# Kernel optimization log

Hardware: AMD Instinct MI355X
Metric: run time of the kernel (lower is better)

## Reference

```python
import jax, jax.numpy as jnp
import numpy as np

# Static problem structure (matches setup_inputs)
B, NPOLY, VPP, L = 32, 256, 64, 32
LAYERS = 3
PLEN = L * 2 ** LAYERS  # 256
LN_EPS = 1e-5


def _layernorm(h, g, b):
    mu = h.mean(-1, keepdims=True)
    var = ((h - mu) ** 2).mean(-1, keepdims=True)
    return g * (h - mu) / jnp.sqrt(var + LN_EPS) + b


def _forward(data, W0, b0, g0, beta0, W1, b1, g1, beta1, W2, b2, g2, beta2,
             Wq, bq, Wk, bk, Wv, bv):
    # row 0 holds agent polyline index in feature 0
    agent_id = data[:, 0, 0].astype(jnp.int32)  # [B]
    vecs = data[:, 1:, :]
    vecs = vecs.at[:, :, -1].set(0.0)  # zero out polyline-id feature (data[:,:,-1]=0)
    x = vecs.reshape(B, NPOLY, VPP, L)  # uniform polyline groups

    # SubGraph: 3 layers of (MLP -> maxpool aggregate -> concat), doubling width
    for (W, b, g, be) in ((W0, b0, g0, beta0), (W1, b1, g1, beta1), (W2, b2, g2, beta2)):
        h = jax.nn.relu(_layernorm(x @ W + b, g, be))  # [B,P,V,c]
        agg = h.max(axis=2, keepdims=True)             # [B,P,1,c]
        x = jnp.concatenate([h, jnp.broadcast_to(agg, h.shape)], axis=-1)  # [B,P,V,2c]
    P = x.max(axis=2)  # [B, NPOLY, PLEN] polyline features

    # Global graph: single-head attention with agent polyline as query
    q = P[jnp.arange(B), agent_id] @ Wq + bq          # [B, C]
    k = P @ Wk + bk                                    # [B, P, C]
    v = P @ Wv + bv
    scores = jnp.einsum('bc,bpc->bp', q, k) / jnp.sqrt(jnp.float32(PLEN))
    att = jax.nn.softmax(scores, axis=-1)
    return jnp.einsum('bp,bpc->bc', att, v)           # [B, PLEN]


def setup_inputs() -> dict:
    key = jax.random.key(0)
    ks = jax.random.split(key, 24)
    V = 1 + NPOLY * VPP
    data = jax.random.normal(ks[0], (B, V, L), dtype=jnp.float32)
    agent = jax.random.randint(ks[1], (B,), 0, NPOLY).astype(jnp.float32)
    data = data.at[:, 0, :].set(0.0).at[:, 0, 0].set(agent)
    pid = jnp.repeat(jnp.arange(NPOLY), VPP).astype(jnp.float32)
    data = data.at[:, 1:, -1].set(pid[None, :])

    inp = {'data': data}
    c = L
    for i in range(LAYERS):
        inp[f'W{i}'] = 0.02 * jax.random.normal(ks[2 + i], (c, c), dtype=jnp.float32)
        inp[f'b{i}'] = jnp.zeros((c,), jnp.float32)
        inp[f'g{i}'] = jnp.ones((c,), jnp.float32)
        inp[f'beta{i}'] = jnp.zeros((c,), jnp.float32)
        c *= 2
    C = PLEN
    for j, nm in enumerate(('q', 'k', 'v')):
        inp[f'W{nm}'] = 0.02 * jax.random.normal(ks[10 + j], (C, C), dtype=jnp.float32)
        inp[f'b{nm}'] = jnp.zeros((C,), jnp.float32)
    return inp


def reference(data, W0, b0, g0, beta0, W1, b1, g1, beta1, W2, b2, g2, beta2,
              Wq, bq, Wk, bk, Wv, bv):
    return _forward(data, W0, b0, g0, beta0, W1, b1, g1, beta1, W2, b2, g2, beta2,
                    Wq, bq, Wk, bk, Wv, bv)
```

## Files before the change

kernel.cpp:

```cpp
#include <hip/hip_runtime.h>

#define NPOLY 256
#define VPP   64
#define LCH   32
#define NV    (1 + NPOLY * VPP)
#define LN_EPS 1e-5f

typedef __bf16 bf16x8 __attribute__((ext_vector_type(8)));
typedef float  f32x4  __attribute__((ext_vector_type(4)));

union U4B8 { uint4 u; bf16x8 v; };

__device__ __forceinline__ unsigned packbf(float a, float b) {
    unsigned r;
    asm("v_cvt_pk_bf16_f32 %0, %1, %2" : "=v"(r) : "v"(a), "v"(b));
    return r;
}

#define DPPF(x, ctrl) __int_as_float(__builtin_amdgcn_update_dpp(0, __float_as_int(x), (ctrl), 0xF, 0xF, true))

__device__ __forceinline__ float red16sum(float x) {
    x += DPPF(x, 0xB1);
    x += DPPF(x, 0x4E);
    x += DPPF(x, 0x141);
    x += DPPF(x, 0x140);
    return x;
}

__global__ void vn_prep(const float* __restrict__ W0, const float* __restrict__ W1,
                        const float* __restrict__ W2,
                        const float* __restrict__ Wq, const float* __restrict__ Wk,
                        const float* __restrict__ Wv,
                        float* __restrict__ Wvf, float* __restrict__ Wqf,
                        float* __restrict__ WkfT, uint4* __restrict__ wpack)
{
    int t = blockIdx.x * 256 + threadIdx.x;
    if (t < 32768) {
        Wvf[t] = Wv[t] + Wv[t + 32768];
        return;
    }
    t -= 32768;
    if (t < 32768) {
        Wqf[t] = Wq[t] + Wq[t + 32768];
        return;
    }
    t -= 32768;
    if (t < 32768) {
        int j = t >> 8, c = t & 255;
        WkfT[c * 128 + j] = Wk[j * 256 + c] + Wk[(j + 128) * 256 + c];
        return;
    }
    t -= 32768;
    if (t < 22 * 64) {
        int f = t >> 6, L = t & 63, q = L >> 4, m = L & 15;
        const float* src; int N, k0, col;
        if (f < 2)      { src = W0; N = 32;  k0 = q * 8;                 col = f * 16 + m; }
        else if (f < 6) { src = W1; N = 64;  k0 = q * 8;                 col = (f - 2) * 16 + m; }
        else { int g = f - 6; src = W2; N = 128; k0 = (g >> 3) * 32 + q * 8; col = (g & 7) * 16 + m; }
        float e[8];
        #pragma unroll
        for (int j = 0; j < 8; j++) e[j] = src[(k0 + j) * N + col];
        uint4 o;
        o.x = packbf(e[0], e[1]); o.y = packbf(e[2], e[3]);
        o.z = packbf(e[4], e[5]); o.w = packbf(e[6], e[7]);
        wpack[f * 64 + L] = o;
    }
}

__global__ __launch_bounds__(256, 3) void vn_mlp(
    const float* __restrict__ data, const uint4* __restrict__ wpack,
    const float* __restrict__ b0, const float* __restrict__ g0, const float* __restrict__ be0,
    const float* __restrict__ W1, const float* __restrict__ b1,
    const float* __restrict__ g1, const float* __restrict__ be1,
    const float* __restrict__ W2, const float* __restrict__ b2,
    const float* __restrict__ g2, const float* __restrict__ be2,
    float* __restrict__ Ph)
{
    __shared__ __align__(16) unsigned short hbuf[64 * 72];
    __shared__ float partA[4][128];
    __shared__ float partB[4][128];

    const int tid = threadIdx.x;
    const int w = tid >> 6, L = tid & 63, q = L >> 4, m = L & 15;
    const int blk = blockIdx.x;
    const int bb = blk >> 8, pp = blk & 255;
    const int r0 = w * 16;

    const float* rowbase = data + ((size_t)bb * NV + 1 + (size_t)pp * VPP) * LCH;
    bf16x8 A0;
    {
        const float* rp = rowbase + (size_t)(r0 + m) * LCH + q * 8;
        float4 u = *(const float4*)rp;
        float4 v = *(const float4*)(rp + 4);
        if (q == 3) v.w = 0.f;
        U4B8 c;
        c.u.x = packbf(u.x, u.y); c.u.y = packbf(u.z, u.w);
        c.u.z = packbf(v.x, v.y); c.u.w = packbf(v.z, v.w);
        A0 = c.v;
    }
    f32x4 acc0[2];
    {
        U4B8 t0, t1; t0.u = wpack[0 * 64 + L]; t1.u = wpack[1 * 64 + L];
        float bca = b0[m], bcb = b0[16 + m];
        f32x4 a0 = { bca, bca, bca, bca };
        f32x4 a1 = { bcb, bcb, bcb, bcb };
        acc0[0] = __builtin_amdgcn_mfma_f32_16x16x32_bf16(A0, t0.v, a0, 0, 0, 0);
        acc0[1] = __builtin_amdgcn_mfma_f32_16x16x32_bf16(A0, t1.v, a1, 0, 0, 0);
    }
    {
        float g0c[2]  = { g0[m],  g0[16 + m]  };
        float be0c[2] = { be0[m], be0[16 + m] };
        float a0mx[2] = { 0.f, 0.f };
        #pragma unroll
        for (int reg = 0; reg < 4; reg++) {
            float x0 = acc0[0][reg], x1 = acc0[1][reg];
            float rs = red16sum(x0 + x1);
            float rq = red16sum(x0 * x0 + x1 * x1);
            float mu = rs * (1.f / 32.f);
            float var = rq * (1.f / 32.f) - mu * mu;
            float ri = rsqrtf(var + LN_EPS);
            #pragma unroll
            for (int ct = 0; ct < 2; ct++) {
                float v = fmaxf(fmaf(g0c[ct] * ri, acc0[ct][reg] - mu, be0c[ct]), 0.f);
                acc0[ct][reg] = v;
                a0mx[ct] = fmaxf(a0mx[ct], v);
            }
        }
        #pragma unroll
        for (int ct = 0; ct < 2; ct++) {
            float v = a0mx[ct];
            v = fmaxf(v, __shfl_xor(v, 16, 64));
            v = fmaxf(v, __shfl_xor(v, 32, 64));
            a0mx[ct] = v;
        }
        if (q == 0) { partA[w][m] = a0mx[0]; partA[w][16 + m] = a0mx[1]; }
    }
    #pragma unroll
    for (int reg = 0; reg < 4; reg++) {
        int row = r0 + q * 4 + reg;
        unsigned u = packbf(acc0[0][reg], acc0[1][reg]);
        hbuf[row * 72 + m]      = (unsigned short)u;
        hbuf[row * 72 + 16 + m] = (unsigned short)(u >> 16);
    }
    __syncthreads();

    {
        float p = 0.f;
        int j0 = w * 8;
        #pragma unroll
        for (int jj = 0; jj < 8; jj++) {
            int j = j0 + jj;
            float a = fmaxf(fmaxf(partA[0][j], partA[1][j]), fmaxf(partA[2][j], partA[3][j]));
            p = fmaf(a, W1[(32 + j) * 64 + L], p);
        }
        partB[w][L] = p;
    }
    __syncthreads();

    bf16x8 A1;
    { U4B8 c; c.u = *(const uint4*)(hbuf + (r0 + m) * 72 + q * 8); A1 = c.v; }
    f32x4 acc1[4];
    #pragma unroll
    for (int ct = 0; ct < 4; ct++) {
        U4B8 wv; wv.u = wpack[(2 + ct) * 64 + L];
        int n = ct * 16 + m;
        float au = b1[n] + ((partB[0][n] + partB[1][n]) + (partB[2][n] + partB[3][n]));
        f32x4 a = { au, au, au, au };
        acc1[ct] = __builtin_amdgcn_mfma_f32_16x16x32_bf16(A1, wv.v, a, 0, 0, 0);
    }
    {
        float g1c[4], be1c[4];
        #pragma unroll
        for (int ct = 0; ct < 4; ct++) { g1c[ct] = g1[ct * 16 + m]; be1c[ct] = be1[ct * 16 + m]; }
        float a1mx[4] = { 0.f, 0.f, 0.f, 0.f };
        #pragma unroll
        for (int reg = 0; reg < 4; reg++) {
            float rs = 0.f, rq = 0.f;
            #pragma unroll
            for (int ct = 0; ct < 4; ct++) { float x = acc1[ct][reg]; rs += x; rq = fmaf(x, x, rq); }
            rs = red16sum(rs);
            rq = red16sum(rq);
            float mu = rs * (1.f / 64.f);
            float var = rq * (1.f / 64.f) - mu * mu;
            float ri = rsqrtf(var + LN_EPS);
            #pragma unroll
            for (int ct = 0; ct < 4; ct++) {
                float v = fmaxf(fmaf(g1c[ct] * ri, acc1[ct][reg] - mu, be1c[ct]), 0.f);
                acc1[ct][reg] = v;
                a1mx[ct] = fmaxf(a1mx[ct], v);
            }
        }
        #pragma unroll
        for (int ct = 0; ct < 4; ct++) {
            float v = a1mx[ct];
            v = fmaxf(v, __shfl_xor(v, 16, 64));
            v = fmaxf(v, __shfl_xor(v, 32, 64));
            a1mx[ct] = v;
        }
        if (q == 0) {
            #pragma unroll
            for (int ct = 0; ct < 4; ct++) partA[w][ct * 16 + m] = a1mx[ct];
        }
    }
    #pragma unroll
    for (int reg = 0; reg < 4; reg++) {
        int row = r0 + q * 4 + reg;
        unsigned ua = packbf(acc1[0][reg], acc1[1][reg]);
        unsigned ub = packbf(acc1[2][reg], acc1[3][reg]);
        hbuf[row * 72 + m]      = (unsigned short)ua;
        hbuf[row * 72 + 16 + m] = (unsigned short)(ua >> 16);
        hbuf[row * 72 + 32 + m] = (unsigned short)ub;
        hbuf[row * 72 + 48 + m] = (unsigned short)(ub >> 16);
    }
    __syncthreads();

    {
        float pa = 0.f, pb = 0.f;
        int j0 = w * 16;
        #pragma unroll
        for (int jj = 0; jj < 16; jj++) {
            int j = j0 + jj;
            float a = fmaxf(fmaxf(partA[0][j], partA[1][j]), fmaxf(partA[2][j], partA[3][j]));
            pa = fmaf(a, W2[(64 + j) * 128 + L],      pa);
            pb = fmaf(a, W2[(64 + j) * 128 + 64 + L], pb);
        }
        partB[w][L]      = pa;
        partB[w][64 + L] = pb;
    }
    __syncthreads();

    bf16x8 A2[2];
    #pragma unroll
    for (int ks = 0; ks < 2; ks++) {
        U4B8 c; c.u = *(const uint4*)(hbuf + (r0 + m) * 72 + ks * 32 + q * 8);
        A2[ks] = c.v;
    }
    f32x4 acc2[8];
    #pragma unroll
    for (int ct = 0; ct < 8; ct++) {
        U4B8 wa, wb;
        wa.u = wpack[(6 + ct) * 64 + L];
        wb.u = wpack[(14 + ct) * 64 + L];
        int n = ct * 16 + m;
        float au = b2[n] + ((partB[0][n] + partB[1][n]) + (partB[2][n] + partB[3][n]));
        f32x4 a = { au, au, au, au };
        a = __builtin_amdgcn_mfma_f32_16x16x32_bf16(A2[0], wa.v, a, 0, 0, 0);
        a = __builtin_amdgcn_mfma_f32_16x16x32_bf16(A2[1], wb.v, a, 0, 0, 0);
        acc2[ct] = a;
    }
    {
        float g2c[8], be2c[8];
        #pragma unroll
        for (int ct = 0; ct < 8; ct++) { g2c[ct] = g2[ct * 16 + m]; be2c[ct] = be2[ct * 16 + m]; }
        float m2[8] = { 0.f, 0.f, 0.f, 0.f, 0.f, 0.f, 0.f, 0.f };
        #pragma unroll
        for (int reg = 0; reg < 4; reg++) {
            float rs = 0.f, rq = 0.f;
            #pragma unroll
            for (int ct = 0; ct < 8; ct++) { float x = acc2[ct][reg]; rs += x; rq = fmaf(x, x, rq); }
            rs = red16sum(rs);
            rq = red16sum(rq);
            float mu = rs * (1.f / 128.f);
            float var = rq * (1.f / 128.f) - mu * mu;
            float ri = rsqrtf(var + LN_EPS);
            #pragma unroll
            for (int ct = 0; ct < 8; ct++) {
                float v = fmaxf(fmaf(g2c[ct] * ri, acc2[ct][reg] - mu, be2c[ct]), 0.f);
                m2[ct] = fmaxf(m2[ct], v);
            }
        }
        #pragma unroll
        for (int ct = 0; ct < 8; ct++) {
            float v = m2[ct];
            v = fmaxf(v, __shfl_xor(v, 16, 64));
            v = fmaxf(v, __shfl_xor(v, 32, 64));
            m2[ct] = v;
        }
        if (q == 0) {
            #pragma unroll
            for (int ct = 0; ct < 8; ct++) partA[w][ct * 16 + m] = m2[ct];
        }
    }
    __syncthreads();

    if (tid < 128) {
        float v = fmaxf(fmaxf(partA[0][tid], partA[1][tid]),
                        fmaxf(partA[2][tid], partA[3][tid]));
        Ph[(size_t)blk * 128 + tid] = v;
    }
}

__global__ __launch_bounds__(256) void vn_attn(
    const float* __restrict__ data, const float* __restrict__ Ph,
    const float* __restrict__ Wqf, const float* __restrict__ WkfT,
    const float* __restrict__ bq,
    const float* __restrict__ Wvf, const float* __restrict__ bv,
    float* __restrict__ out)
{
    extern __shared__ float shPh[];
    __shared__ __align__(16) float qs[256], tts[128], att[256], pb[128];
    __shared__ __align__(16) float part[256];
    __shared__ float red[8];
    const int b = blockIdx.x, tid = threadIdx.x, lane = tid & 63, wave = tid >> 6;
    const float* PhB = Ph + (size_t)b * NPOLY * 128;
    const int agent = (int)data[(size_t)b * NV * LCH];

    {
        const float4* src = (const float4*)PhB;
        #pragma unroll
        for (int it = 0; it < 32; it++) {
            int idx4 = it * 256 + tid;
            float4 v = src[idx4];
            int lin = idx4 * 4;
            int p = lin >> 7, c = lin & 127;
            float* dst = shPh + p * 129 + c;
            dst[0] = v.x; dst[1] = v.y; dst[2] = v.z; dst[3] = v.w;
        }
    }
    __syncthreads();

    {
        const int c = tid;
        const float* pa = shPh + agent * 129;
        float s0 = bq[c], s1 = 0.f, s2 = 0.f, s3 = 0.f;
        for (int i = 0; i < 128; i += 4) {
            s0 = fmaf(pa[i],     Wqf[(i)     * 256 + c], s0);
            s1 = fmaf(pa[i + 1], Wqf[(i + 1) * 256 + c], s1);
            s2 = fmaf(pa[i + 2], Wqf[(i + 2) * 256 + c], s2);
            s3 = fmaf(pa[i + 3], Wqf[(i + 3) * 256 + c], s3);
        }
        qs[c] = (s0 + s1) + (s2 + s3);
    }
    __syncthreads();

    {
        const int j = tid & 127, h = tid >> 7;
        const float* wk = WkfT + (size_t)(h * 128) * 128 + j;
        const float* qp = qs + h * 128;
        float s0 = 0.f, s1 = 0.f, s2 = 0.f, s3 = 0.f;
        for (int c = 0; c < 128; c += 4) {
            s0 = fmaf(qp[c],     wk[(c)     * 128], s0);
            s1 = fmaf(qp[c + 1], wk[(c + 1) * 128], s1);
            s2 = fmaf(qp[c + 2], wk[(c + 2) * 128], s2);
            s3 = fmaf(qp[c + 3], wk[(c + 3) * 128], s3);
        }
        part[tid] = (s0 + s1) + (s2 + s3);
    }
    __syncthreads();
    if (tid < 128) tts[tid] = part[tid] + part[128 + tid];
    __syncthreads();

    float sv;
    {
        const float* prl = shPh + tid * 129;
        float s0 = 0.f, s1 = 0.f, s2 = 0.f, s3 = 0.f;
        #pragma unroll
        for (int j = 0; j < 128; j += 4) {
            s0 = fmaf(prl[j],     tts[j],     s0);
            s1 = fmaf(prl[j + 1], tts[j + 1], s1);
            s2 = fmaf(prl[j + 2], tts[j + 2], s2);
            s3 = fmaf(prl[j + 3], tts[j + 3], s3);
        }
        sv = ((s0 + s1) + (s2 + s3)) * 0.0625f;
    }
    float mx = sv;
    #pragma unroll
    for (int s = 1; s < 64; s <<= 1) mx = fmaxf(mx, __shfl_xor(mx, s, 64));
    if (lane == 0) red[wave] = mx;
    __syncthreads();
    mx = fmaxf(fmaxf(red[0], red[1]), fmaxf(red[2], red[3]));
    float e = expf(sv - mx);
    float sm = e;
    #pragma unroll
    for (int s = 1; s < 64; s <<= 1) sm += __shfl_xor(sm, s, 64);
    if (lane == 0) red[4 + wave] = sm;
    __syncthreads();
    const float tot = red[4] + red[5] + red[6] + red[7];
    att[tid] = e / tot;
    __syncthreads();

    {
        const int c = tid & 127, h = tid >> 7;
        const float* ap = att + h * 128;
        const float* pp = shPh + (size_t)(h * 128) * 129 + c;
        float s0 = 0.f, s1 = 0.f, s2 = 0.f, s3 = 0.f;
        #pragma unroll
        for (int p = 0; p < 128; p += 4) {
            s0 = fmaf(ap[p],     pp[(p)     * 129], s0);
            s1 = fmaf(ap[p + 1], pp[(p + 1) * 129], s1);
            s2 = fmaf(ap[p + 2], pp[(p + 2) * 129], s2);
            s3 = fmaf(ap[p + 3], pp[(p + 3) * 129], s3);
        }
        part[tid] = (s0 + s1) + (s2 + s3);
    }
    __syncthreads();
    if (tid < 128) pb[tid] = part[tid] + part[128 + tid];
    __syncthreads();

    {
        const float* wv = Wvf + tid;
        float s0 = 0.f, s1 = 0.f, s2 = 0.f, s3 = 0.f;
        #pragma unroll
        for (int j = 0; j < 128; j += 4) {
            s0 = fmaf(pb[j],     wv[(j)     * 256], s0);
            s1 = fmaf(pb[j + 1], wv[(j + 1) * 256], s1);
            s2 = fmaf(pb[j + 2], wv[(j + 2) * 256], s2);
            s3 = fmaf(pb[j + 3], wv[(j + 3) * 256], s3);
        }
        out[(size_t)b * 256 + tid] = bv[tid] + ((s0 + s1) + (s2 + s3));
    }
}

extern "C" void kernel_launch(void* const* d_in, const int* in_sizes, int n_in,
                              void* d_out, int out_size, void* d_ws, size_t ws_size,
                              hipStream_t stream)
{
    const float* data = (const float*)d_in[0];
    const float* W0 = (const float*)d_in[1];
    const float* b0 = (const float*)d_in[2];
    const float* g0 = (const float*)d_in[3];
    const float* be0= (const float*)d_in[4];
    const float* W1 = (const float*)d_in[5];
    const float* b1 = (const float*)d_in[6];
    const float* g1 = (const float*)d_in[7];
    const float* be1= (const float*)d_in[8];
    const float* W2 = (const float*)d_in[9];
    const float* b2 = (const float*)d_in[10];
    const float* g2 = (const float*)d_in[11];
    const float* be2= (const float*)d_in[12];
    const float* Wq = (const float*)d_in[13];
    const float* bq = (const float*)d_in[14];
    const float* Wk = (const float*)d_in[15];
    const float* bk = (const float*)d_in[16];
    const float* Wv = (const float*)d_in[17];
    const float* bv = (const float*)d_in[18];
    (void)bk;

    char* wsb = (char*)d_ws;
    float* Ph    = (float*)(wsb);
    float* Wqf   = (float*)(wsb + 4194304);
    float* WkfT  = (float*)(wsb + 4325376);
    float* Wvf   = (float*)(wsb + 4456448);
    uint4* wpack = (uint4*)(wsb + 4653568);

    static int attn_attr_set = 0;
    if (!attn_attr_set) {
        hipFuncSetAttribute((const void*)vn_attn,
                            hipFuncAttributeMaxDynamicSharedMemorySize, 132096);
        attn_attr_set = 1;
    }

    vn_prep<<<390, 256, 0, stream>>>(W0, W1, W2, Wq, Wk, Wv, Wvf, Wqf, WkfT, wpack);
    vn_mlp<<<32 * NPOLY, 256, 0, stream>>>(data, wpack,
                                           b0, g0, be0,
                                           W1, b1, g1, be1,
                                           W2, b2, g2, be2, Ph);
    vn_attn<<<32, 256, 132096, stream>>>(data, Ph, Wqf, WkfT, bq, Wvf, bv, (float*)d_out);
}
```

Before: 189.9 us.

## Split attention kernel across 8 blocks per batch and precompute max aggregates

```diff
diff --git a/kernel.cpp b/kernel.cpp
--- a/kernel.cpp
+++ b/kernel.cpp
@@ -79,6 +79,7 @@
     __shared__ __align__(16) unsigned short hbuf[64 * 72];
     __shared__ float partA[4][128];
     __shared__ float partB[4][128];
+    __shared__ float agg0[32], agg1[64];
 
     const int tid = threadIdx.x;
     const int w = tid >> 6, L = tid & 63, q = L >> 4, m = L & 15;
@@ -143,6 +144,10 @@
         hbuf[row * 72 + 16 + m] = (unsigned short)(u >> 16);
     }
     __syncthreads();
+    if (tid < 32)
+        agg0[tid] = fmaxf(fmaxf(partA[0][tid], partA[1][tid]),
+                          fmaxf(partA[2][tid], partA[3][tid]));
+    __syncthreads();
 
     {
         float p = 0.f;
@@ -150,8 +155,7 @@
         #pragma unroll
         for (int jj = 0; jj < 8; jj++) {
             int j = j0 + jj;
-            float a = fmaxf(fmaxf(partA[0][j], partA[1][j]), fmaxf(partA[2][j], partA[3][j]));
-            p = fmaf(a, W1[(32 + j) * 64 + L], p);
+            p = fmaf(agg0[j], W1[(32 + j) * 64 + L], p);
         }
         partB[w][L] = p;
     }
@@ -213,6 +217,10 @@
         hbuf[row * 72 + 48 + m] = (unsigned short)(ub >> 16);
     }
     __syncthreads();
+    if (tid < 64)
+        agg1[tid] = fmaxf(fmaxf(partA[0][tid], partA[1][tid]),
+                          fmaxf(partA[2][tid], partA[3][tid]));
+    __syncthreads();
 
     {
         float pa = 0.f, pb = 0.f;
@@ -220,7 +228,7 @@
         #pragma unroll
         for (int jj = 0; jj < 16; jj++) {
             int j = j0 + jj;
-            float a = fmaxf(fmaxf(partA[0][j], partA[1][j]), fmaxf(partA[2][j], partA[3][j]));
+            float a = agg1[j];
             pa = fmaf(a, W2[(64 + j) * 128 + L],      pa);
             pb = fmaf(a, W2[(64 + j) * 128 + 64 + L], pb);
         }
@@ -301,7 +309,8 @@
     __shared__ __align__(16) float qs[256], tts[128], att[256], pb[128];
     __shared__ __align__(16) float part[256];
     __shared__ float red[8];
-    const int b = blockIdx.x, tid = threadIdx.x, lane = tid & 63, wave = tid >> 6;
+    const int bg = blockIdx.x, b = bg >> 3, g = bg & 7;
+    const int tid = threadIdx.x, lane = tid & 63, wave = tid >> 6;
     const float* PhB = Ph + (size_t)b * NPOLY * 128;
     const int agent = (int)data[(size_t)b * NV * LCH];
 
@@ -398,16 +407,23 @@
     __syncthreads();
 
     {
-        const float* wv = Wvf + tid;
-        float s0 = 0.f, s1 = 0.f, s2 = 0.f, s3 = 0.f;
-        #pragma unroll
-        for (int j = 0; j < 128; j += 4) {
-            s0 = fmaf(pb[j],     wv[(j)     * 256], s0);
-            s1 = fmaf(pb[j + 1], wv[(j + 1) * 256], s1);
-            s2 = fmaf(pb[j + 2], wv[(j + 2) * 256], s2);
-            s3 = fmaf(pb[j + 3], wv[(j + 3) * 256], s3);
-        }
-        out[(size_t)b * 256 + tid] = bv[tid] + ((s0 + s1) + (s2 + s3));
+        const int c32 = tid & 31, jg = tid >> 5;
+        const float* wv = Wvf + g * 32 + c32;
+        const int j0 = jg * 16;
+        float s0 = 0.f, s1 = 0.f;
+        #pragma unroll
+        for (int jj = 0; jj < 16; jj += 2) {
+            s0 = fmaf(pb[j0 + jj],     wv[(j0 + jj)     * 256], s0);
+            s1 = fmaf(pb[j0 + jj + 1], wv[(j0 + jj + 1) * 256], s1);
+        }
+        part[tid] = s0 + s1;
+    }
+    __syncthreads();
+    if (tid < 32) {
+        float s = bv[g * 32 + tid];
+        #pragma unroll
+        for (int k = 0; k < 8; k++) s += part[k * 32 + tid];
+        out[(size_t)b * 256 + g * 32 + tid] = s;
     }
 }
 
@@ -455,5 +471,5 @@
                                            b0, g0, be0,
                                            W1, b1, g1, be1,
                                            W2, b2, g2, be2, Ph);
-    vn_attn<<<32, 256, 132096, stream>>>(data, Ph, Wqf, WkfT, bq, Wvf, bv, (float*)d_out);
-}
+    vn_attn<<<32 * 8, 256, 132096, stream>>>(data, Ph, Wqf, WkfT, bq, Wvf, bv, (float*)d_out);
+}
```

New measurement: 189.2 us. Within noise of the previous version (-0.3%).

## Split attention kernel reductions across 1024 threads with partial sums

Applied to the files above, without the earlier changes.

```diff
diff --git a/kernel.cpp b/kernel.cpp
--- a/kernel.cpp
+++ b/kernel.cpp
@@ -290,7 +290,7 @@
     }
 }
 
-__global__ __launch_bounds__(256) void vn_attn(
+__global__ __launch_bounds__(1024) void vn_attn(
     const float* __restrict__ data, const float* __restrict__ Ph,
     const float* __restrict__ Wqf, const float* __restrict__ WkfT,
     const float* __restrict__ bq,
@@ -298,18 +298,18 @@
     float* __restrict__ out)
 {
     extern __shared__ float shPh[];
-    __shared__ __align__(16) float qs[256], tts[128], att[256], pb[128];
-    __shared__ __align__(16) float part[256];
+    __shared__ __align__(16) float qs[256], tts[128], att[256], pb[128], sc[256];
+    __shared__ __align__(16) float part[1024];
     __shared__ float red[8];
-    const int b = blockIdx.x, tid = threadIdx.x, lane = tid & 63, wave = tid >> 6;
+    const int b = blockIdx.x, tid = threadIdx.x;
     const float* PhB = Ph + (size_t)b * NPOLY * 128;
     const int agent = (int)data[(size_t)b * NV * LCH];
 
     {
         const float4* src = (const float4*)PhB;
         #pragma unroll
-        for (int it = 0; it < 32; it++) {
-            int idx4 = it * 256 + tid;
+        for (int it = 0; it < 8; it++) {
+            int idx4 = it * 1024 + tid;
             float4 v = src[idx4];
             int lin = idx4 * 4;
             int p = lin >> 7, c = lin & 127;
@@ -320,95 +320,126 @@
     __syncthreads();
 
     {
-        const int c = tid;
-        const float* pa = shPh + agent * 129;
-        float s0 = bq[c], s1 = 0.f, s2 = 0.f, s3 = 0.f;
-        for (int i = 0; i < 128; i += 4) {
-            s0 = fmaf(pa[i],     Wqf[(i)     * 256 + c], s0);
-            s1 = fmaf(pa[i + 1], Wqf[(i + 1) * 256 + c], s1);
-            s2 = fmaf(pa[i + 2], Wqf[(i + 2) * 256 + c], s2);
-            s3 = fmaf(pa[i + 3], Wqf[(i + 3) * 256 + c], s3);
-        }
-        qs[c] = (s0 + s1) + (s2 + s3);
-    }
-    __syncthreads();
-
-    {
-        const int j = tid & 127, h = tid >> 7;
-        const float* wk = WkfT + (size_t)(h * 128) * 128 + j;
-        const float* qp = qs + h * 128;
+        const int c = tid & 255, ig = tid >> 8;
+        const float* pa = shPh + agent * 129 + ig * 32;
+        const float* wq = Wqf + (size_t)(ig * 32) * 256 + c;
         float s0 = 0.f, s1 = 0.f, s2 = 0.f, s3 = 0.f;
-        for (int c = 0; c < 128; c += 4) {
+        #pragma unroll
+        for (int i = 0; i < 32; i += 4) {
+            s0 = fmaf(pa[i],     wq[(i)     * 256], s0);
+            s1 = fmaf(pa[i + 1], wq[(i + 1) * 256], s1);
+            s2 = fmaf(pa[i + 2], wq[(i + 2) * 256], s2);
+            s3 = fmaf(pa[i + 3], wq[(i + 3) * 256], s3);
+        }
+        part[ig * 256 + c] = (s0 + s1) + (s2 + s3);
+    }
+    __syncthreads();
+    if (tid < 256)
+        qs[tid] = bq[tid] + ((part[tid] + part[256 + tid]) + (part[512 + tid] + part[768 + tid]));
+    __syncthreads();
+
+    {
+        const int j = tid & 127, cg = tid >> 7;
+        const float* wk = WkfT + (size_t)(cg * 32) * 128 + j;
+        const float* qp = qs + cg * 32;
+        float s0 = 0.f, s1 = 0.f, s2 = 0.f, s3 = 0.f;
+        #pragma unroll
+        for (int c = 0; c < 32; c += 4) {
             s0 = fmaf(qp[c],     wk[(c)     * 128], s0);
             s1 = fmaf(qp[c + 1], wk[(c + 1) * 128], s1);
             s2 = fmaf(qp[c + 2], wk[(c + 2) * 128], s2);
             s3 = fmaf(qp[c + 3], wk[(c + 3) * 128], s3);
         }
-        part[tid] = (s0 + s1) + (s2 + s3);
-    }
-    __syncthreads();
-    if (tid < 128) tts[tid] = part[tid] + part[128 + tid];
-    __syncthreads();
-
-    float sv;
-    {
-        const float* prl = shPh + tid * 129;
+        part[cg * 128 + j] = (s0 + s1) + (s2 + s3);
+    }
+    __syncthreads();
+    if (tid < 128) {
+        float s = 0.f;
+        #pragma unroll
+        for (int k = 0; k < 8; k++) s += part[k * 128 + tid];
+        tts[tid] = s;
+    }
+    __syncthreads();
+
+    {
+        const int p = tid & 255, jg = tid >> 8;
+        const float* prl = shPh + p * 129 + jg * 32;
+        const float* tp = tts + jg * 32;
         float s0 = 0.f, s1 = 0.f, s2 = 0.f, s3 = 0.f;
         #pragma unroll
-        for (int j = 0; j < 128; j += 4) {
-            s0 = fmaf(prl[j],     tts[j],     s0);
-            s1 = fmaf(prl[j + 1], tts[j + 1], s1);
-            s2 = fmaf(prl[j + 2], tts[j + 2], s2);
-            s3 = fmaf(prl[j + 3], tts[j + 3], s3);
-        }
-        sv = ((s0 + s1) + (s2 + s3)) * 0.0625f;
-    }
-    float mx = sv;
+        for (int j = 0; j < 32; j += 4) {
+            s0 = fmaf(prl[j],     tp[j],     s0);
+            s1 = fmaf(prl[j + 1], tp[j + 1], s1);
+            s2 = fmaf(prl[j + 2], tp[j + 2], s2);
+            s3 = fmaf(prl[j + 3], tp[j + 3], s3);
+        }
+        part[jg * 256 + p] = (s0 + s1) + (s2 + s3);
+    }
+    __syncthreads();
+    if (tid < 256)
+        sc[tid] = ((part[tid] + part[256 + tid]) + (part[512 + tid] + part[768 + tid])) * 0.0625f;
+    __syncthreads();
+
+    float svv = sc[tid & 255];
+    float mx = svv;
     #pragma unroll
     for (int s = 1; s < 64; s <<= 1) mx = fmaxf(mx, __shfl_xor(mx, s, 64));
-    if (lane == 0) red[wave] = mx;
+    if (tid < 256 && (tid & 63) == 0) red[tid >> 6] = mx;
     __syncthreads();
     mx = fmaxf(fmaxf(red[0], red[1]), fmaxf(red[2], red[3]));
-    float e = expf(sv - mx);
+    float e = expf(svv - mx);
     float sm = e;
     #pragma unroll
     for (int s = 1; s < 64; s <<= 1) sm += __shfl_xor(sm, s, 64);
-    if (lane == 0) red[4 + wave] = sm;
-    __syncthreads();
-    const float tot = red[4] + red[5] + red[6] + red[7];
-    att[tid] = e / tot;
-    __syncthreads();
-
-    {
-        const int c = tid & 127, h = tid >> 7;
-        const float* ap = att + h * 128;
-        const float* pp = shPh + (size_t)(h * 128) * 129 + c;
+    if (tid < 256 && (tid & 63) == 0) red[4 + (tid >> 6)] = sm;
+    __syncthreads();
+    {
+        const float tot = red[4] + red[5] + red[6] + red[7];
+        if (tid < 256) att[tid] = e / tot;
+    }
+    __syncthreads();
+
+    {
+        const int c = tid & 127, pg = tid >> 7;
+        const float* ap = att + pg * 32;
+        const float* pp = shPh + (size_t)(pg * 32) * 129 + c;
         float s0 = 0.f, s1 = 0.f, s2 = 0.f, s3 = 0.f;
         #pragma unroll
-        for (int p = 0; p < 128; p += 4) {
+        for (int p = 0; p < 32; p += 4) {
             s0 = fmaf(ap[p],     pp[(p)     * 129], s0);
             s1 = fmaf(ap[p + 1], pp[(p + 1) * 129], s1);
             s2 = fmaf(ap[p + 2], pp[(p + 2) * 129], s2);
             s3 = fmaf(ap[p + 3], pp[(p + 3) * 129], s3);
         }
-        part[tid] = (s0 + s1) + (s2 + s3);
-    }
-    __syncthreads();
-    if (tid < 128) pb[tid] = part[tid] + part[128 + tid];
-    __syncthreads();
-
-    {
-        const float* wv = Wvf + tid;
+        part[pg * 128 + c] = (s0 + s1) + (s2 + s3);
+    }
+    __syncthreads();
+    if (tid < 128) {
+        float s = 0.f;
+        #pragma unroll
+        for (int k = 0; k < 8; k++) s += part[k * 128 + tid];
+        pb[tid] = s;
+    }
+    __syncthreads();
+
+    {
+        const int c = tid & 255, jg = tid >> 8;
+        const float* wv = Wvf + (size_t)(jg * 32) * 256 + c;
+        const float* pbp = pb + jg * 32;
         float s0 = 0.f, s1 = 0.f, s2 = 0.f, s3 = 0.f;
         #pragma unroll
-        for (int j = 0; j < 128; j += 4) {
-            s0 = fmaf(pb[j],     wv[(j)     * 256], s0);
-            s1 = fmaf(pb[j + 1], wv[(j + 1) * 256], s1);
-            s2 = fmaf(pb[j + 2], wv[(j + 2) * 256], s2);
-            s3 = fmaf(pb[j + 3], wv[(j + 3) * 256], s3);
-        }
-        out[(size_t)b * 256 + tid] = bv[tid] + ((s0 + s1) + (s2 + s3));
-    }
+        for (int j = 0; j < 32; j += 4) {
+            s0 = fmaf(pbp[j],     wv[(j)     * 256], s0);
+            s1 = fmaf(pbp[j + 1], wv[(j + 1) * 256], s1);
+            s2 = fmaf(pbp[j + 2], wv[(j + 2) * 256], s2);
+            s3 = fmaf(pbp[j + 3], wv[(j + 3) * 256], s3);
+        }
+        part[jg * 256 + c] = (s0 + s1) + (s2 + s3);
+    }
+    __syncthreads();
+    if (tid < 256)
+        out[(size_t)b * 256 + tid] =
+            bv[tid] + ((part[tid] + part[256 + tid]) + (part[512 + tid] + part[768 + tid]));
 }
 
 extern "C" void kernel_launch(void* const* d_in, const int* in_sizes, int n_in,
@@ -455,5 +486,5 @@
                                            b0, g0, be0,
                                            W1, b1, g1, be1,
                                            W2, b2, g2, be2, Ph);
-    vn_attn<<<32, 256, 132096, stream>>>(data, Ph, Wqf, WkfT, bq, Wvf, bv, (float*)d_out);
-}
+    vn_attn<<<32, 1024, 132096, stream>>>(data, Ph, Wqf, WkfT, bq, Wvf, bv, (float*)d_out);
+}
```

After: 188.4 us. About the same (-0.8%).
